# Kernel tuning notes

Measured on AMD Instinct MI355X. Metric: run time of the kernel, lower is better.

Reference implementation:

```python
import jax, jax.numpy as jnp
import numpy as np

N, E, IN_DIM, HID = 50000, 800000, 512, 256
EPS = 1e-5


def _gat_layer(x, W, a_src, a_dst, b, src, dst, n, heads, ch):
    # x: [N, F_in] -> h: [N, H, C]
    h = (x @ W).reshape(n, heads, ch)
    alpha_src = jnp.sum(h * a_src, axis=-1)  # [N, H]
    alpha_dst = jnp.sum(h * a_dst, axis=-1)  # [N, H]
    e = jax.nn.leaky_relu(alpha_src[src] + alpha_dst[dst], negative_slope=0.2)  # [E', H]
    # segment softmax over incoming edges of each destination node
    m = jax.ops.segment_max(e, dst, num_segments=n)  # [N, H]
    ex = jnp.exp(e - m[dst])
    den = jax.ops.segment_sum(ex, dst, num_segments=n)  # [N, H]
    alpha = ex / den[dst]
    out = jax.ops.segment_sum(alpha[:, :, None] * h[src], dst, num_segments=n)  # [N, H, C]
    return out.reshape(n, heads * ch) + b


def _layer_norm(x, w, b):
    mu = jnp.mean(x, axis=-1, keepdims=True)
    var = jnp.mean(jnp.square(x - mu), axis=-1, keepdims=True)
    return (x - mu) * jax.lax.rsqrt(var + EPS) * w + b


def setup_inputs() -> dict:
    key = jax.random.key(0)
    ks = jax.random.split(key, 16)
    d = {}
    d['x'] = jax.random.normal(ks[0], (N, IN_DIM), dtype=jnp.float32)
    d['edge_index'] = jax.random.randint(ks[1], (2, E), 0, N, dtype=jnp.int32)
    s = 0.05
    # layer 0: GATConv(512, 64, heads=4)
    d['W0'] = jax.random.normal(ks[2], (IN_DIM, HID), dtype=jnp.float32) * s
    d['as0'] = jax.random.normal(ks[3], (4, 64), dtype=jnp.float32) * s
    d['ad0'] = jax.random.normal(ks[4], (4, 64), dtype=jnp.float32) * s
    d['b0'] = jnp.zeros((HID,), dtype=jnp.float32)
    d['lnw0'] = jnp.ones((HID,), dtype=jnp.float32)
    d['lnb0'] = jnp.zeros((HID,), dtype=jnp.float32)
    # layer 1: GATConv(256, 64, heads=4)
    d['W1'] = jax.random.normal(ks[5], (HID, HID), dtype=jnp.float32) * s
    d['as1'] = jax.random.normal(ks[6], (4, 64), dtype=jnp.float32) * s
    d['ad1'] = jax.random.normal(ks[7], (4, 64), dtype=jnp.float32) * s
    d['b1'] = jnp.zeros((HID,), dtype=jnp.float32)
    d['lnw1'] = jnp.ones((HID,), dtype=jnp.float32)
    d['lnb1'] = jnp.zeros((HID,), dtype=jnp.float32)
    # layer 2: GATConv(256, 256, heads=1)
    d['W2'] = jax.random.normal(ks[8], (HID, HID), dtype=jnp.float32) * s
    d['as2'] = jax.random.normal(ks[9], (1, HID), dtype=jnp.float32) * s
    d['ad2'] = jax.random.normal(ks[10], (1, HID), dtype=jnp.float32) * s
    d['b2'] = jnp.zeros((HID,), dtype=jnp.float32)
    d['lnw2'] = jnp.ones((HID,), dtype=jnp.float32)
    d['lnb2'] = jnp.zeros((HID,), dtype=jnp.float32)
    return d


def reference(x, edge_index, W0, as0, ad0, b0, lnw0, lnb0,
              W1, as1, ad1, b1, lnw1, lnb1,
              W2, as2, ad2, b2, lnw2, lnb2):
    n = x.shape[0]
    loop = jnp.arange(n, dtype=edge_index.dtype)
    src = jnp.concatenate([edge_index[0], loop])  # PyG add_self_loops=True
    dst = jnp.concatenate([edge_index[1], loop])
    h = _gat_layer(x, W0, as0, ad0, b0, src, dst, n, 4, 64)
    h = jax.nn.elu(_layer_norm(h, lnw0, lnb0))
    h = _gat_layer(h, W1, as1, ad1, b1, src, dst, n, 4, 64)
    h = jax.nn.elu(_layer_norm(h, lnw1, lnb1))
    h = _gat_layer(h, W2, as2, ad2, b2, src, dst, n, 1, HID)
    h = jax.nn.elu(_layer_norm(h, lnw2, lnb2))
    return h
```

## Files before the change

### kernel.cpp

```cpp
#include <hip/hip_runtime.h>

#define HID 256
#define EPSV 1e-5f
#define ASTR 136
#define BSTR 72

typedef __bf16 bf16x8 __attribute__((ext_vector_type(8)));
typedef float  floatx4 __attribute__((ext_vector_type(4)));

static __device__ __forceinline__ ushort f2bf(float f) {
  union { float f; unsigned int i; } c; c.f = f;
  unsigned int u = c.i;
  u += 0x7FFFu + ((u >> 16) & 1u);
  return (ushort)(u >> 16);
}
static __device__ __forceinline__ float bf2f(ushort u) {
  union { unsigned int i; float f; } c; c.i = ((unsigned int)u) << 16; return c.f;
}

__global__ void count_kernel(const int* __restrict__ ei, int* __restrict__ deg, int E, int tot) {
  int i = blockIdx.x * blockDim.x + threadIdx.x;
  if (i < tot) {
    int dst = (i < E) ? ei[E + i] : (i - E);
    atomicAdd(&deg[dst], 1);
  }
}

__global__ void scanA_kernel(const int* __restrict__ deg, int* __restrict__ incl,
                             int* __restrict__ sums, int n) {
  __shared__ int buf[1024];
  const int t = threadIdx.x;
  const int i = blockIdx.x * 1024 + t;
  int x = (i < n) ? deg[i] : 0;
  buf[t] = x;
  __syncthreads();
  for (int off = 1; off < 1024; off <<= 1) {
    int v = (t >= off) ? buf[t - off] : 0;
    __syncthreads();
    buf[t] += v;
    __syncthreads();
  }
  if (i < n) incl[i] = buf[t];
  if (t == 1023) sums[blockIdx.x] = buf[1023];
}

__global__ void scanB_kernel(int* __restrict__ sums, int* __restrict__ offs, int nblk) {
  __shared__ int buf[256];
  const int t = threadIdx.x;
  int x = (t < nblk) ? sums[t] : 0;
  buf[t] = x;
  __syncthreads();
  for (int off = 1; off < 256; off <<= 1) {
    int v = (t >= off) ? buf[t - off] : 0;
    __syncthreads();
    buf[t] += v;
    __syncthreads();
  }
  if (t < nblk) offs[t] = buf[t] - x;
  if (t == nblk) offs[nblk] = buf[nblk - 1];
}

__global__ void scanC_kernel(const int* __restrict__ deg, const int* __restrict__ incl,
                             const int* __restrict__ offs, int* __restrict__ rp,
                             int* __restrict__ cur, int n, int nblk) {
  const int i = blockIdx.x * 1024 + threadIdx.x;
  if (i < n) {
    int v = offs[blockIdx.x] + incl[i] - deg[i];
    rp[i] = v;
    cur[i] = v;
  }
  if (i == 0) rp[n] = offs[nblk];
}

__global__ void scatter_kernel(const int* __restrict__ ei, int* __restrict__ cur,
                               int* __restrict__ csr, int E, int tot) {
  int i = blockIdx.x * blockDim.x + threadIdx.x;
  if (i < tot) {
    int src = (i < E) ? ei[i] : (i - E);
    int dst = (i < E) ? ei[E + i] : (i - E);
    int pos = atomicAdd(&cur[dst], 1);
    csr[pos] = src;
  }
}

__global__ __launch_bounds__(256) void transpose_kernel(
    const float* __restrict__ W, ushort* __restrict__ Wt, int K) {
  __shared__ ushort tile[32][33];
  const int tx = threadIdx.x & 31, ty = threadIdx.x >> 5;
  const int bm = blockIdx.x * 32;
  const int bk = blockIdx.y * 32;
  #pragma unroll
  for (int yy = ty; yy < 32; yy += 8)
    tile[tx][yy] = f2bf(W[(size_t)(bk + yy) * 256 + bm + tx]);
  __syncthreads();
  #pragma unroll
  for (int yy = ty; yy < 32; yy += 8)
    Wt[(size_t)(bm + yy) * K + bk + tx] = tile[yy][tx];
}

static __device__ __forceinline__ void alpha_epilogue(
    const floatx4 (&acc)[4][4], const float* __restrict__ avs,
    const float* __restrict__ avd, float* __restrict__ asrc,
    float* __restrict__ adst, int row0, int col0, int wm, int wn,
    int quad, int m16, int nrows) {
  float sv[4], dv[4];
  #pragma unroll
  for (int j = 0; j < 4; j++) {
    int col = col0 + wn + j * 16 + m16;
    sv[j] = avs[col];
    dv[j] = avd[col];
  }
  const int idx = (col0 + wn) >> 6;
  #pragma unroll
  for (int i = 0; i < 4; i++) {
    #pragma unroll
    for (int r = 0; r < 4; r++) {
      int row = row0 + wm + i * 16 + quad * 4 + r;
      float s = 0.f, d = 0.f;
      #pragma unroll
      for (int j = 0; j < 4; j++) {
        s = fmaf(acc[i][j][r], sv[j], s);
        d = fmaf(acc[i][j][r], dv[j], d);
      }
      #pragma unroll
      for (int o = 1; o < 16; o <<= 1) { s += __shfl_xor(s, o); d += __shfl_xor(d, o); }
      if (m16 == 0 && row < nrows) {
        asrc[row * 4 + idx] = s;
        adst[row * 4 + idx] = d;
      }
    }
  }
}

__global__ __launch_bounds__(256) void gemm_kernel(
    const float* __restrict__ A, const ushort* __restrict__ Bt,
    ushort* __restrict__ hb, const float* __restrict__ avs,
    const float* __restrict__ avd, float* __restrict__ asrc,
    float* __restrict__ adst, int nrows, int K) {
  __shared__ ushort At[128 * ASTR];
  __shared__ ushort Bs[128 * BSTR];
  const int tid  = threadIdx.x;
  const int lane = tid & 63;
  const int wave = tid >> 6;
  const int quad = lane >> 4;
  const int m16  = lane & 15;
  const int row0 = blockIdx.x * 128;
  const int col0 = blockIdx.y * 128;
  const int wm = (wave >> 1) * 64;
  const int wn = (wave & 1) * 64;

  floatx4 acc[4][4];
  #pragma unroll
  for (int i = 0; i < 4; i++)
    #pragma unroll
    for (int j = 0; j < 4; j++) acc[i][j] = (floatx4){0.f, 0.f, 0.f, 0.f};

  const int arow = tid >> 3;
  const int acol = (tid & 7) * 4;
  const int brow = tid >> 2;
  const int bcol = (tid & 3) * 8;

  for (int k0 = 0; k0 < K; k0 += 64) {
    floatx4 va[4][2];
    int4 vb[2][2];
    #pragma unroll
    for (int i = 0; i < 4; i++) {
      int ar = min(row0 + arow + 32 * i, nrows - 1);
      #pragma unroll
      for (int c = 0; c < 2; c++)
        va[i][c] = *(const floatx4*)(A + (size_t)ar * K + k0 + c * 32 + acol);
    }
    #pragma unroll
    for (int i = 0; i < 2; i++) {
      int r = brow + 64 * i;
      #pragma unroll
      for (int c = 0; c < 2; c++)
        vb[i][c] = *(const int4*)(Bt + (size_t)(col0 + r) * K + k0 + c * 32 + bcol);
    }
    #pragma unroll
    for (int i = 0; i < 4; i++) {
      int r = arow + 32 * i;
      #pragma unroll
      for (int c = 0; c < 2; c++) {
        floatx4 v = va[i][c];
        unsigned u0 = __float_as_uint(v[0]), u1 = __float_as_uint(v[1]);
        unsigned u2 = __float_as_uint(v[2]), u3 = __float_as_uint(v[3]);
        unsigned ph0 = __builtin_amdgcn_perm(u1, u0, 0x07060302u);
        unsigned ph1 = __builtin_amdgcn_perm(u3, u2, 0x07060302u);
        float l0 = v[0] - __uint_as_float(u0 & 0xffff0000u);
        float l1 = v[1] - __uint_as_float(u1 & 0xffff0000u);
        float l2 = v[2] - __uint_as_float(u2 & 0xffff0000u);
        float l3 = v[3] - __uint_as_float(u3 & 0xffff0000u);
        unsigned pl0 = __builtin_amdgcn_perm(__float_as_uint(l1), __float_as_uint(l0), 0x07060302u);
        unsigned pl1 = __builtin_amdgcn_perm(__float_as_uint(l3), __float_as_uint(l2), 0x07060302u);
        *(uint2*)&At[r * ASTR + c * 32 + acol]      = make_uint2(ph0, ph1);
        *(uint2*)&At[r * ASTR + 64 + c * 32 + acol] = make_uint2(pl0, pl1);
      }
    }
    #pragma unroll
    for (int i = 0; i < 2; i++) {
      int r = brow + 64 * i;
      #pragma unroll
      for (int c = 0; c < 2; c++)
        *(int4*)&Bs[r * BSTR + c * 32 + bcol] = vb[i][c];
    }
    __syncthreads();
    #pragma unroll
    for (int kk = 0; kk < 2; kk++) {
      bf16x8 bfr[4];
      #pragma unroll
      for (int j = 0; j < 4; j++)
        bfr[j] = *(const bf16x8*)&Bs[(wn + j * 16 + m16) * BSTR + kk * 32 + quad * 8];
      #pragma unroll
      for (int p = 0; p < 2; p++) {
        bf16x8 af[4];
        #pragma unroll
        for (int i = 0; i < 4; i++)
          af[i] = *(const bf16x8*)&At[(wm + i * 16 + m16) * ASTR + p * 64 + kk * 32 + quad * 8];
        #pragma unroll
        for (int i = 0; i < 4; i++)
          #pragma unroll
          for (int j = 0; j < 4; j++)
            acc[i][j] = __builtin_amdgcn_mfma_f32_16x16x32_bf16(af[i], bfr[j], acc[i][j], 0, 0, 0);
      }
    }
    __syncthreads();
  }
  #pragma unroll
  for (int i = 0; i < 4; i++) {
    int rbase = row0 + wm + i * 16 + quad * 4;
    #pragma unroll
    for (int j = 0; j < 4; j++) {
      int col = col0 + wn + j * 16 + m16;
      #pragma unroll
      for (int r = 0; r < 4; r++) {
        int row = rbase + r;
        if (row < nrows) hb[(size_t)row * HID + col] = f2bf(acc[i][j][r]);
      }
    }
  }
  alpha_epilogue(acc, avs, avd, asrc, adst, row0, col0, wm, wn, quad, m16, nrows);
}

__global__ __launch_bounds__(256) void gemm_packed_kernel(
    const ushort* __restrict__ A, const ushort* __restrict__ Bt,
    ushort* __restrict__ hb, const float* __restrict__ avs,
    const float* __restrict__ avd, float* __restrict__ asrc,
    float* __restrict__ adst, int nrows) {
  __shared__ ushort At[128 * BSTR];
  __shared__ ushort Bs[128 * BSTR];
  const int tid  = threadIdx.x;
  const int lane = tid & 63;
  const int wave = tid >> 6;
  const int quad = lane >> 4;
  const int m16  = lane & 15;
  const int row0 = blockIdx.x * 128;
  const int col0 = blockIdx.y * 128;
  const int wm = (wave >> 1) * 64;
  const int wn = (wave & 1) * 64;

  floatx4 acc[4][4];
  #pragma unroll
  for (int i = 0; i < 4; i++)
    #pragma unroll
    for (int j = 0; j < 4; j++) acc[i][j] = (floatx4){0.f, 0.f, 0.f, 0.f};

  const int srow = tid >> 2;
  const int scol = (tid & 3) * 8;

  for (int k0 = 0; k0 < 512; k0 += 64) {
    const int kb = k0 & 255;
    int4 va[2][2], vb[2][2];
    #pragma unroll
    for (int i = 0; i < 2; i++) {
      int r = srow + 64 * i;
      int ar = min(row0 + r, nrows - 1);
      #pragma unroll
      for (int c = 0; c < 2; c++) {
        va[i][c] = *(const int4*)(A + (size_t)ar * 512 + k0 + c * 32 + scol);
        vb[i][c] = *(const int4*)(Bt + (size_t)(col0 + r) * 256 + kb + c * 32 + scol);
      }
    }
    #pragma unroll
    for (int i = 0; i < 2; i++) {
      int r = srow + 64 * i;
      #pragma unroll
      for (int c = 0; c < 2; c++) {
        *(int4*)&At[r * BSTR + c * 32 + scol] = va[i][c];
        *(int4*)&Bs[r * BSTR + c * 32 + scol] = vb[i][c];
      }
    }
    __syncthreads();
    #pragma unroll
    for (int kk = 0; kk < 2; kk++) {
      bf16x8 af[4], bfr[4];
      #pragma unroll
      for (int j = 0; j < 4; j++)
        bfr[j] = *(const bf16x8*)&Bs[(wn + j * 16 + m16) * BSTR + kk * 32 + quad * 8];
      #pragma unroll
      for (int i = 0; i < 4; i++)
        af[i] = *(const bf16x8*)&At[(wm + i * 16 + m16) * BSTR + kk * 32 + quad * 8];
      #pragma unroll
      for (int i = 0; i < 4; i++)
        #pragma unroll
        for (int j = 0; j < 4; j++)
          acc[i][j] = __builtin_amdgcn_mfma_f32_16x16x32_bf16(af[i], bfr[j], acc[i][j], 0, 0, 0);
    }
    __syncthreads();
  }
  #pragma unroll
  for (int i = 0; i < 4; i++) {
    int rbase = row0 + wm + i * 16 + quad * 4;
    #pragma unroll
    for (int j = 0; j < 4; j++) {
      int col = col0 + wn + j * 16 + m16;
      #pragma unroll
      for (int r = 0; r < 4; r++) {
        int row = rbase + r;
        if (row < nrows) hb[(size_t)row * HID + col] = f2bf(acc[i][j][r]);
      }
    }
  }
  alpha_epilogue(acc, avs, avd, asrc, adst, row0, col0, wm, wn, quad, m16, nrows);
}

__global__ __launch_bounds__(256) void agg_ln_kernel(
    const ushort* __restrict__ hb, const float* __restrict__ asrc,
    const float* __restrict__ adst, const int* __restrict__ rp,
    const int* __restrict__ csr,
    const float* __restrict__ bias, const float* __restrict__ lnw,
    const float* __restrict__ lnb, ushort* __restrict__ apk,
    float* __restrict__ fout, int H, int n) {
  __shared__ float2 exs[4][64];
  const int t = threadIdx.x;
  const int w = t >> 6, lane = t & 63;
  const int nid = blockIdx.x * 4 + w;
  if (nid >= n) return;
  const int CH = (H == 4) ? 16 : 64;
  const int jj = lane & (CH - 1);
  const int hh = (H == 4) ? (lane >> 4) : 0;
  const int ch = 4 * lane;
  float ad;
  if (H == 4) {
    ad = adst[nid * 4 + hh];
  } else {
    floatx4 t4 = *(const floatx4*)(adst + nid * 4);
    ad = t4[0] + t4[1] + t4[2] + t4[3];
  }
  const int beg = rp[nid], end = rp[nid + 1];
  const char* hbase = (const char*)hb + ch * 2;
  float den = 0.f;
  float a0 = 0.f, a1 = 0.f, a2 = 0.f, a3 = 0.f;
  float b0 = 0.f, b1 = 0.f, b2 = 0.f, b3 = 0.f;
  float c0_ = 0.f, c1 = 0.f, c2 = 0.f, c3 = 0.f;
  float d0_ = 0.f, d1 = 0.f, d2 = 0.f, d3 = 0.f;

  int snext = 0;
  {
    int cnt0 = min(CH, end - beg);
    if (lane < cnt0) snext = csr[beg + lane];
  }

  for (int c0 = beg; c0 < end; c0 += CH) {
    const int cnt = min(CH, end - c0);
    int s = snext;
    const int nc0 = c0 + CH;
    if (nc0 < end) {
      int ncnt = min(CH, end - nc0);
      if (lane < ncnt) snext = csr[nc0 + lane];
    }
    s = __shfl(s, jj);
    float ex = 0.f;
    if (jj < cnt) {
      float e;
      if (H == 4) {
        e = asrc[s * 4 + hh] + ad;
      } else {
        floatx4 t4 = *(const floatx4*)(asrc + s * 4);
        e = t4[0] + t4[1] + t4[2] + t4[3] + ad;
      }
      e = (e > 0.f) ? e : 0.2f * e;
      ex = __expf(fminf(e, 60.f));
    }
    exs[w][lane] = make_float2(ex, __int_as_float(s << 9));
    float dsum = ex;
    #pragma unroll
    for (int o = 32; o > 0; o >>= 1)
      if (o < CH) dsum += __shfl_xor(dsum, o);
    den += dsum;
    const float2* exw = &exs[w][hh * CH];
    int j = 0;
    for (; j + 4 <= cnt; j += 4) {
      float2 q0 = exw[j];
      float2 q1 = exw[j + 1];
      float2 q2 = exw[j + 2];
      float2 q3 = exw[j + 3];
      uint2 u0 = *(const uint2*)(hbase + __float_as_int(q0.y));
      uint2 u1 = *(const uint2*)(hbase + __float_as_int(q1.y));
      uint2 u2 = *(const uint2*)(hbase + __float_as_int(q2.y));
      uint2 u3 = *(const uint2*)(hbase + __float_as_int(q3.y));
      a0 = fmaf(q0.x, __uint_as_float(u0.x << 16), a0);
      a1 = fmaf(q0.x, __uint_as_float(u0.x & 0xffff0000u), a1);
      a2 = fmaf(q0.x, __uint_as_float(u0.y << 16), a2);
      a3 = fmaf(q0.x, __uint_as_float(u0.y & 0xffff0000u), a3);
      b0 = fmaf(q1.x, __uint_as_float(u1.x << 16), b0);
      b1 = fmaf(q1.x, __uint_as_float(u1.x & 0xffff0000u), b1);
      b2 = fmaf(q1.x, __uint_as_float(u1.y << 16), b2);
      b3 = fmaf(q1.x, __uint_as_float(u1.y & 0xffff0000u), b3);
      c0_ = fmaf(q2.x, __uint_as_float(u2.x << 16), c0_);
      c1 = fmaf(q2.x, __uint_as_float(u2.x & 0xffff0000u), c1);
      c2 = fmaf(q2.x, __uint_as_float(u2.y << 16), c2);
      c3 = fmaf(q2.x, __uint_as_float(u2.y & 0xffff0000u), c3);
      d0_ = fmaf(q3.x, __uint_as_float(u3.x << 16), d0_);
      d1 = fmaf(q3.x, __uint_as_float(u3.x & 0xffff0000u), d1);
      d2 = fmaf(q3.x, __uint_as_float(u3.y << 16), d2);
      d3 = fmaf(q3.x, __uint_as_float(u3.y & 0xffff0000u), d3);
    }
    for (; j < cnt; ++j) {
      float2 q0 = exw[j];
      uint2 u0 = *(const uint2*)(hbase + __float_as_int(q0.y));
      a0 = fmaf(q0.x, __uint_as_float(u0.x << 16), a0);
      a1 = fmaf(q0.x, __uint_as_float(u0.x & 0xffff0000u), a1);
      a2 = fmaf(q0.x, __uint_as_float(u0.y << 16), a2);
      a3 = fmaf(q0.x, __uint_as_float(u0.y & 0xffff0000u), a3);
    }
  }
  a0 += b0 + c0_ + d0_;
  a1 += b1 + c1 + d1;
  a2 += b2 + c2 + d2;
  a3 += b3 + c3 + d3;

  const float inv = 1.f / den;
  const floatx4 bia = *(const floatx4*)(bias + ch);
  float v0 = a0 * inv + bia[0];
  float v1 = a1 * inv + bia[1];
  float v2 = a2 * inv + bia[2];
  float v3 = a3 * inv + bia[3];
  float r1 = v0 + v1 + v2 + v3;
  #pragma unroll
  for (int o = 32; o > 0; o >>= 1) r1 += __shfl_xor(r1, o);
  float mu = r1 * (1.f / HID);
  float e0 = v0 - mu, e1 = v1 - mu, e2 = v2 - mu, e3 = v3 - mu;
  float r2 = e0 * e0 + e1 * e1 + e2 * e2 + e3 * e3;
  #pragma unroll
  for (int o = 32; o > 0; o >>= 1) r2 += __shfl_xor(r2, o);
  float rstd = rsqrtf(r2 * (1.f / HID) + EPSV);
  const floatx4 wv = *(const floatx4*)(lnw + ch);
  const floatx4 bv = *(const floatx4*)(lnb + ch);
  float y0 = e0 * rstd * wv[0] + bv[0];
  float y1 = e1 * rstd * wv[1] + bv[1];
  float y2 = e2 * rstd * wv[2] + bv[2];
  float y3 = e3 * rstd * wv[3] + bv[3];
  float o0 = (y0 > 0.f) ? y0 : expm1f(y0);
  float o1 = (y1 > 0.f) ? y1 : expm1f(y1);
  float o2 = (y2 > 0.f) ? y2 : expm1f(y2);
  float o3 = (y3 > 0.f) ? y3 : expm1f(y3);
  if (apk) {
    union { ushort us[4]; unsigned long long u64; } ph, pl;
    ushort h0 = f2bf(o0), h1 = f2bf(o1), h2 = f2bf(o2), h3 = f2bf(o3);
    ph.us[0] = h0; ph.us[1] = h1; ph.us[2] = h2; ph.us[3] = h3;
    pl.us[0] = f2bf(o0 - bf2f(h0)); pl.us[1] = f2bf(o1 - bf2f(h1));
    pl.us[2] = f2bf(o2 - bf2f(h2)); pl.us[3] = f2bf(o3 - bf2f(h3));
    *(unsigned long long*)(apk + (size_t)nid * 512 + ch)       = ph.u64;
    *(unsigned long long*)(apk + (size_t)nid * 512 + 256 + ch) = pl.u64;
  } else {
    floatx4 ov; ov[0] = o0; ov[1] = o1; ov[2] = o2; ov[3] = o3;
    *(floatx4*)(fout + (size_t)nid * HID + ch) = ov;
  }
}

extern "C" void kernel_launch(void* const* d_in, const int* in_sizes, int n_in,
                              void* d_out, int out_size, void* d_ws, size_t ws_size,
                              hipStream_t stream) {
  const float* x  = (const float*)d_in[0];
  const int*   ei = (const int*)d_in[1];
  const float* Wm[3]  = {(const float*)d_in[2], (const float*)d_in[8],  (const float*)d_in[14]};
  const float* Avs[3] = {(const float*)d_in[3], (const float*)d_in[9],  (const float*)d_in[15]};
  const float* Avd[3] = {(const float*)d_in[4], (const float*)d_in[10], (const float*)d_in[16]};
  const float* Bia[3] = {(const float*)d_in[5], (const float*)d_in[11], (const float*)d_in[17]};
  const float* Lnw[3] = {(const float*)d_in[6], (const float*)d_in[12], (const float*)d_in[18]};
  const float* Lnb[3] = {(const float*)d_in[7], (const float*)d_in[13], (const float*)d_in[19]};
  const int n = in_sizes[0] / 512;
  const int E = in_sizes[1] / 2;
  const int tot = E + n;
  const int nblk = (n + 1023) / 1024;

  char* p = (char*)d_ws;
  ushort* hb   = (ushort*)p; p += (size_t)n * HID * 2;
  ushort* apk  = (ushort*)p; p += (size_t)n * 512 * 2;
  ushort* Wt   = (ushort*)p; p += 256 * 512 * 2;
  float*  asrc = (float*)p;  p += (size_t)n * 4 * 4;
  float*  adst = (float*)p;  p += (size_t)n * 4 * 4;
  int* rp   = (int*)p; p += (size_t)(n + 1) * 4;
  int* cur  = (int*)p; p += (size_t)n * 4;
  int* csr  = (int*)p; p += (size_t)tot * 4;
  int* deg  = (int*)p; p += (size_t)n * 4;
  int* incl = (int*)p; p += (size_t)n * 4;
  int* sums = (int*)p; p += (size_t)(nblk + 1) * 4;
  int* offs = (int*)p; p += (size_t)(nblk + 1) * 4;

  hipMemsetAsync(deg, 0, (size_t)n * 4, stream);
  count_kernel<<<(tot + 255) / 256, 256, 0, stream>>>(ei, deg, E, tot);
  scanA_kernel<<<nblk, 1024, 0, stream>>>(deg, incl, sums, n);
  scanB_kernel<<<1, 256, 0, stream>>>(sums, offs, nblk);
  scanC_kernel<<<nblk, 1024, 0, stream>>>(deg, incl, offs, rp, cur, n, nblk);
  scatter_kernel<<<(tot + 255) / 256, 256, 0, stream>>>(ei, cur, csr, E, tot);

  const int KB[3] = {512, 256, 256};
  const int HH[3] = {4, 4, 1};
  dim3 gg((n + 127) / 128, 2);
  for (int l = 0; l < 3; l++) {
    dim3 tg(8, KB[l] / 32);
    transpose_kernel<<<tg, 256, 0, stream>>>(Wm[l], Wt, KB[l]);
    if (l == 0)
      gemm_kernel<<<gg, 256, 0, stream>>>(x, Wt, hb, Avs[l], Avd[l], asrc, adst, n, 512);
    else
      gemm_packed_kernel<<<gg, 256, 0, stream>>>(apk, Wt, hb, Avs[l], Avd[l], asrc, adst, n);
    agg_ln_kernel<<<(n + 3) / 4, 256, 0, stream>>>(
        hb, asrc, adst, rp, csr, Bia[l], Lnw[l], Lnb[l],
        (l < 2) ? apk : (ushort*)nullptr,
        (l == 2) ? (float*)d_out : (float*)nullptr, HH[l], n);
  }
}
```

Baseline: 617.3 us.

## Use direct global-to-LDS loads in GEMMs and simplify aggregation loop

Both GEMM kernels now stage operand tiles with global_load_lds (16-byte direct-to-LDS loads) instead of loading into registers and writing to shared memory. The padded LDS stride is dropped to an unpadded 64, which avoids register staging but may add bank conflicts on the MFMA fragment reads. The aggregation kernel loses its CSR index prefetch and its 4-way unroll goes down to 2-way, reducing register pressure at the cost of memory-level parallelism. All three weight transposes are now hoisted ahead of the layer loop into separate buffers.

```diff
diff --git a/kernel.cpp b/kernel.cpp
--- a/kernel.cpp
+++ b/kernel.cpp
@@ -3,10 +3,15 @@
 #define HID 256
 #define EPSV 1e-5f
 #define ASTR 136
-#define BSTR 72
 
 typedef __bf16 bf16x8 __attribute__((ext_vector_type(8)));
 typedef float  floatx4 __attribute__((ext_vector_type(4)));
+
+typedef __attribute__((address_space(3))) unsigned char lds_uc;
+typedef __attribute__((address_space(1))) const unsigned char gbl_uc;
+static __device__ __forceinline__ void gl_lds16(const void* g, void* l) {
+  __builtin_amdgcn_global_load_lds((gbl_uc*)g, (lds_uc*)l, 16, 0, 0);
+}
 
 static __device__ __forceinline__ ushort f2bf(float f) {
   union { float f; unsigned int i; } c; c.f = f;
@@ -138,7 +143,7 @@
     const float* __restrict__ avd, float* __restrict__ asrc,
     float* __restrict__ adst, int nrows, int K) {
   __shared__ ushort At[128 * ASTR];
-  __shared__ ushort Bs[128 * BSTR];
+  __shared__ ushort Bs[128 * 64];
   const int tid  = threadIdx.x;
   const int lane = tid & 63;
   const int wave = tid >> 6;
@@ -157,32 +162,23 @@
 
   const int arow = tid >> 3;
   const int acol = (tid & 7) * 4;
-  const int brow = tid >> 2;
-  const int bcol = (tid & 3) * 8;
+  const int grow = lane >> 3;
+  const int gcol = (lane & 7) * 8;
 
   for (int k0 = 0; k0 < K; k0 += 64) {
-    floatx4 va[4][2];
-    int4 vb[2][2];
+    #pragma unroll
+    for (int i = 0; i < 4; i++) {
+      int r = wave * 32 + i * 8 + grow;
+      gl_lds16(Bt + (size_t)(col0 + r) * K + k0 + gcol,
+               Bs + (wave * 32 + i * 8) * 64);
+    }
     #pragma unroll
     for (int i = 0; i < 4; i++) {
       int ar = min(row0 + arow + 32 * i, nrows - 1);
-      #pragma unroll
-      for (int c = 0; c < 2; c++)
-        va[i][c] = *(const floatx4*)(A + (size_t)ar * K + k0 + c * 32 + acol);
-    }
-    #pragma unroll
-    for (int i = 0; i < 2; i++) {
-      int r = brow + 64 * i;
-      #pragma unroll
-      for (int c = 0; c < 2; c++)
-        vb[i][c] = *(const int4*)(Bt + (size_t)(col0 + r) * K + k0 + c * 32 + bcol);
-    }
-    #pragma unroll
-    for (int i = 0; i < 4; i++) {
       int r = arow + 32 * i;
       #pragma unroll
       for (int c = 0; c < 2; c++) {
-        floatx4 v = va[i][c];
+        floatx4 v = *(const floatx4*)(A + (size_t)ar * K + k0 + c * 32 + acol);
         unsigned u0 = __float_as_uint(v[0]), u1 = __float_as_uint(v[1]);
         unsigned u2 = __float_as_uint(v[2]), u3 = __float_as_uint(v[3]);
         unsigned ph0 = __builtin_amdgcn_perm(u1, u0, 0x07060302u);
@@ -197,20 +193,13 @@
         *(uint2*)&At[r * ASTR + 64 + c * 32 + acol] = make_uint2(pl0, pl1);
       }
     }
-    #pragma unroll
-    for (int i = 0; i < 2; i++) {
-      int r = brow + 64 * i;
-      #pragma unroll
-      for (int c = 0; c < 2; c++)
-        *(int4*)&Bs[r * BSTR + c * 32 + bcol] = vb[i][c];
-    }
     __syncthreads();
     #pragma unroll
     for (int kk = 0; kk < 2; kk++) {
       bf16x8 bfr[4];
       #pragma unroll
       for (int j = 0; j < 4; j++)
-        bfr[j] = *(const bf16x8*)&Bs[(wn + j * 16 + m16) * BSTR + kk * 32 + quad * 8];
+        bfr[j] = *(const bf16x8*)&Bs[(wn + j * 16 + m16) * 64 + kk * 32 + quad * 8];
       #pragma unroll
       for (int p = 0; p < 2; p++) {
         bf16x8 af[4];
@@ -247,8 +236,8 @@
     ushort* __restrict__ hb, const float* __restrict__ avs,
     const float* __restrict__ avd, float* __restrict__ asrc,
     float* __restrict__ adst, int nrows) {
-  __shared__ ushort At[128 * BSTR];
-  __shared__ ushort Bs[128 * BSTR];
+  __shared__ ushort At[128 * 64];
+  __shared__ ushort Bs[128 * 64];
   const int tid  = threadIdx.x;
   const int lane = tid & 63;
   const int wave = tid >> 6;
@@ -265,30 +254,19 @@
     #pragma unroll
     for (int j = 0; j < 4; j++) acc[i][j] = (floatx4){0.f, 0.f, 0.f, 0.f};
 
-  const int srow = tid >> 2;
-  const int scol = (tid & 3) * 8;
+  const int grow = lane >> 3;
+  const int gcol = (lane & 7) * 8;
 
   for (int k0 = 0; k0 < 512; k0 += 64) {
     const int kb = k0 & 255;
-    int4 va[2][2], vb[2][2];
-    #pragma unroll
-    for (int i = 0; i < 2; i++) {
-      int r = srow + 64 * i;
+    #pragma unroll
+    for (int i = 0; i < 4; i++) {
+      int r = wave * 32 + i * 8 + grow;
       int ar = min(row0 + r, nrows - 1);
-      #pragma unroll
-      for (int c = 0; c < 2; c++) {
-        va[i][c] = *(const int4*)(A + (size_t)ar * 512 + k0 + c * 32 + scol);
-        vb[i][c] = *(const int4*)(Bt + (size_t)(col0 + r) * 256 + kb + c * 32 + scol);
-      }
-    }
-    #pragma unroll
-    for (int i = 0; i < 2; i++) {
-      int r = srow + 64 * i;
-      #pragma unroll
-      for (int c = 0; c < 2; c++) {
-        *(int4*)&At[r * BSTR + c * 32 + scol] = va[i][c];
-        *(int4*)&Bs[r * BSTR + c * 32 + scol] = vb[i][c];
-      }
+      gl_lds16(A + (size_t)ar * 512 + k0 + gcol,
+               At + (wave * 32 + i * 8) * 64);
+      gl_lds16(Bt + (size_t)(col0 + r) * 256 + kb + gcol,
+               Bs + (wave * 32 + i * 8) * 64);
     }
     __syncthreads();
     #pragma unroll
@@ -296,10 +274,10 @@
       bf16x8 af[4], bfr[4];
       #pragma unroll
       for (int j = 0; j < 4; j++)
-        bfr[j] = *(const bf16x8*)&Bs[(wn + j * 16 + m16) * BSTR + kk * 32 + quad * 8];
+        bfr[j] = *(const bf16x8*)&Bs[(wn + j * 16 + m16) * 64 + kk * 32 + quad * 8];
       #pragma unroll
       for (int i = 0; i < 4; i++)
-        af[i] = *(const bf16x8*)&At[(wm + i * 16 + m16) * BSTR + kk * 32 + quad * 8];
+        af[i] = *(const bf16x8*)&At[(wm + i * 16 + m16) * 64 + kk * 32 + quad * 8];
       #pragma unroll
       for (int i = 0; i < 4; i++)
         #pragma unroll
@@ -352,23 +330,10 @@
   float den = 0.f;
   float a0 = 0.f, a1 = 0.f, a2 = 0.f, a3 = 0.f;
   float b0 = 0.f, b1 = 0.f, b2 = 0.f, b3 = 0.f;
-  float c0_ = 0.f, c1 = 0.f, c2 = 0.f, c3 = 0.f;
-  float d0_ = 0.f, d1 = 0.f, d2 = 0.f, d3 = 0.f;
-
-  int snext = 0;
-  {
-    int cnt0 = min(CH, end - beg);
-    if (lane < cnt0) snext = csr[beg + lane];
-  }
 
   for (int c0 = beg; c0 < end; c0 += CH) {
     const int cnt = min(CH, end - c0);
-    int s = snext;
-    const int nc0 = c0 + CH;
-    if (nc0 < end) {
-      int ncnt = min(CH, end - nc0);
-      if (lane < ncnt) snext = csr[nc0 + lane];
-    }
+    int s = (lane < cnt) ? csr[c0 + lane] : 0;
     s = __shfl(s, jj);
     float ex = 0.f;
     if (jj < cnt) {
@@ -390,15 +355,11 @@
     den += dsum;
     const float2* exw = &exs[w][hh * CH];
     int j = 0;
-    for (; j + 4 <= cnt; j += 4) {
+    for (; j + 2 <= cnt; j += 2) {
       float2 q0 = exw[j];
       float2 q1 = exw[j + 1];
-      float2 q2 = exw[j + 2];
-      float2 q3 = exw[j + 3];
       uint2 u0 = *(const uint2*)(hbase + __float_as_int(q0.y));
       uint2 u1 = *(const uint2*)(hbase + __float_as_int(q1.y));
-      uint2 u2 = *(const uint2*)(hbase + __float_as_int(q2.y));
-      uint2 u3 = *(const uint2*)(hbase + __float_as_int(q3.y));
       a0 = fmaf(q0.x, __uint_as_float(u0.x << 16), a0);
       a1 = fmaf(q0.x, __uint_as_float(u0.x & 0xffff0000u), a1);
       a2 = fmaf(q0.x, __uint_as_float(u0.y << 16), a2);
@@ -407,16 +368,8 @@
       b1 = fmaf(q1.x, __uint_as_float(u1.x & 0xffff0000u), b1);
       b2 = fmaf(q1.x, __uint_as_float(u1.y << 16), b2);
       b3 = fmaf(q1.x, __uint_as_float(u1.y & 0xffff0000u), b3);
-      c0_ = fmaf(q2.x, __uint_as_float(u2.x << 16), c0_);
-      c1 = fmaf(q2.x, __uint_as_float(u2.x & 0xffff0000u), c1);
-      c2 = fmaf(q2.x, __uint_as_float(u2.y << 16), c2);
-      c3 = fmaf(q2.x, __uint_as_float(u2.y & 0xffff0000u), c3);
-      d0_ = fmaf(q3.x, __uint_as_float(u3.x << 16), d0_);
-      d1 = fmaf(q3.x, __uint_as_float(u3.x & 0xffff0000u), d1);
-      d2 = fmaf(q3.x, __uint_as_float(u3.y << 16), d2);
-      d3 = fmaf(q3.x, __uint_as_float(u3.y & 0xffff0000u), d3);
-    }
-    for (; j < cnt; ++j) {
+    }
+    if (j < cnt) {
       float2 q0 = exw[j];
       uint2 u0 = *(const uint2*)(hbase + __float_as_int(q0.y));
       a0 = fmaf(q0.x, __uint_as_float(u0.x << 16), a0);
@@ -425,10 +378,7 @@
       a3 = fmaf(q0.x, __uint_as_float(u0.y & 0xffff0000u), a3);
     }
   }
-  a0 += b0 + c0_ + d0_;
-  a1 += b1 + c1 + d1;
-  a2 += b2 + c2 + d2;
-  a3 += b3 + c3 + d3;
+  a0 += b0; a1 += b1; a2 += b2; a3 += b3;
 
   const float inv = 1.f / den;
   const floatx4 bia = *(const floatx4*)(bias + ch);
@@ -488,7 +438,9 @@
   char* p = (char*)d_ws;
   ushort* hb   = (ushort*)p; p += (size_t)n * HID * 2;
   ushort* apk  = (ushort*)p; p += (size_t)n * 512 * 2;
-  ushort* Wt   = (ushort*)p; p += 256 * 512 * 2;
+  ushort* Wt0  = (ushort*)p; p += 256 * 512 * 2;
+  ushort* Wt1  = (ushort*)p; p += 256 * 256 * 2;
+  ushort* Wt2  = (ushort*)p; p += 256 * 256 * 2;
   float*  asrc = (float*)p;  p += (size_t)n * 4 * 4;
   float*  adst = (float*)p;  p += (size_t)n * 4 * 4;
   int* rp   = (int*)p; p += (size_t)(n + 1) * 4;
@@ -498,6 +450,7 @@
   int* incl = (int*)p; p += (size_t)n * 4;
   int* sums = (int*)p; p += (size_t)(nblk + 1) * 4;
   int* offs = (int*)p; p += (size_t)(nblk + 1) * 4;
+  ushort* Wts[3] = {Wt0, Wt1, Wt2};
 
   hipMemsetAsync(deg, 0, (size_t)n * 4, stream);
   count_kernel<<<(tot + 255) / 256, 256, 0, stream>>>(ei, deg, E, tot);
@@ -508,14 +461,16 @@
 
   const int KB[3] = {512, 256, 256};
   const int HH[3] = {4, 4, 1};
+  for (int l = 0; l < 3; l++) {
+    dim3 tg(8, KB[l] / 32);
+    transpose_kernel<<<tg, 256, 0, stream>>>(Wm[l], Wts[l], KB[l]);
+  }
   dim3 gg((n + 127) / 128, 2);
   for (int l = 0; l < 3; l++) {
-    dim3 tg(8, KB[l] / 32);
-    transpose_kernel<<<tg, 256, 0, stream>>>(Wm[l], Wt, KB[l]);
     if (l == 0)
-      gemm_kernel<<<gg, 256, 0, stream>>>(x, Wt, hb, Avs[l], Avd[l], asrc, adst, n, 512);
+      gemm_kernel<<<gg, 256, 0, stream>>>(x, Wts[0], hb, Avs[l], Avd[l], asrc, adst, n, 512);
     else
-      gemm_packed_kernel<<<gg, 256, 0, stream>>>(apk, Wt, hb, Avs[l], Avd[l], asrc, adst, n);
+      gemm_packed_kernel<<<gg, 256, 0, stream>>>(apk, Wts[l], hb, Avs[l], Avd[l], asrc, adst, n);
     agg_ln_kernel<<<(n + 3) / 4, 256, 0, stream>>>(
         hb, asrc, adst, rp, csr, Bia[l], Lnw[l], Lnb[l],
         (l < 2) ? apk : (ushort*)nullptr,
```

New measurement: 633.6 us. 1.03x slower.
